# Performance work log

Measured on AMD Instinct MI355X. Metric: run time of the kernel, lower is better.

## Reference

```python
import jax, jax.numpy as jnp
import numpy as np

B, T, DIM, HEADS, DH, MLP = 2, 1024, 768, 8, 96, 3072
EPS = 1e-6


def _rms_norm(x, w):
    return x * jax.lax.rsqrt(jnp.mean(x * x, axis=-1, keepdims=True) + EPS) * w


def _rotate_half(x):
    x1, x2 = jnp.split(x, 2, axis=-1)
    return jnp.concatenate([-x2, x1], axis=-1)


def _l2norm(x):
    n = jnp.sqrt(jnp.sum(x * x, axis=-1, keepdims=True))
    return x / jnp.maximum(n, 1e-12)


def setup_inputs() -> dict:
    key = jax.random.key(0)
    ks = jax.random.split(key, 16)
    def rn(k, shape, s=0.02):
        return jax.random.normal(k, shape, jnp.float32) * s
    return {
        'x_stream1': jax.random.normal(ks[0], (B, T, DIM), jnp.float32),
        'x_stream2': jax.random.normal(ks[1], (B, T, DIM), jnp.float32),
        'p_emb': jax.random.normal(ks[2], (B, 1, 1024), jnp.float32),
        'mod_w1': rn(ks[3], (1024, 512)), 'mod_b1': jnp.zeros((512,), jnp.float32),
        'mod_w2': rn(ks[4], (512, DIM * 12)), 'mod_b2': jnp.zeros((DIM * 12,), jnp.float32),
        'norm11_w': jnp.ones((DIM,), jnp.float32), 'norm12_w': jnp.ones((DIM,), jnp.float32),
        'qkv_w': rn(ks[5], (DIM, 3 * DIM)), 'qkv_b': jnp.zeros((3 * DIM,), jnp.float32),
        'qkv2_w': rn(ks[6], (DIM, 3 * DIM)), 'qkv2_b': jnp.zeros((3 * DIM,), jnp.float32),
        'qk_scale': jnp.full((DH,), 10.0, jnp.float32),
        'out_w': rn(ks[7], (DIM, DIM)), 'out_b': jnp.zeros((DIM,), jnp.float32),
        'norm21_w': jnp.ones((DIM,), jnp.float32), 'norm22_w': jnp.ones((DIM,), jnp.float32),
        'mlp1_w1': rn(ks[8], (DIM, MLP)), 'mlp1_b1': jnp.zeros((MLP,), jnp.float32),
        'mlp1_w2': rn(ks[9], (MLP, DIM)), 'mlp1_b2': jnp.zeros((DIM,), jnp.float32),
        'mlp2_w1': rn(ks[10], (DIM, MLP)), 'mlp2_b1': jnp.zeros((MLP,), jnp.float32),
        'mlp2_w2': rn(ks[11], (MLP, DIM)), 'mlp2_b2': jnp.zeros((DIM,), jnp.float32),
    }


def _forward(x_stream1, x_stream2, p_emb, mod_w1, mod_b1, mod_w2, mod_b2,
             norm11_w, norm12_w, qkv_w, qkv_b, qkv2_w, qkv2_b, qk_scale,
             out_w, out_b, norm21_w, norm22_w,
             mlp1_w1, mlp1_b1, mlp1_w2, mlp1_b2,
             mlp2_w1, mlp2_b1, mlp2_w2, mlp2_b2):
    Bc, Tc, D = x_stream1.shape
    # modulation MLP: SiLU -> Linear -> SiLU -> Linear -> 12 chunks of [B, D]
    h = jax.nn.silu(p_emb[:, 0, :])
    h = jax.nn.silu(h @ mod_w1 + mod_b1)
    mod = h @ mod_w2 + mod_b2
    (m1s, m1h, m1g, m2s, m2h, m2g,
     m3s, m3h, m3g, m4s, m4h, m4g) = [m[:, None, :] for m in jnp.split(mod, 12, axis=1)]

    xm1 = _rms_norm(x_stream1, norm11_w) * (1 + m1s) + m1h
    xm2 = _rms_norm(x_stream2, norm12_w) * (1 + m2s) + m2h

    q1, k1, v1 = jnp.split(xm1 @ qkv_w + qkv_b, 3, axis=-1)
    q2, k2, v2 = jnp.split(xm2 @ qkv2_w + qkv2_b, 3, axis=-1)
    q = jnp.concatenate([q1, q2], axis=1)  # [B, 2T, D]
    k = jnp.concatenate([k1, k2], axis=1)
    v = jnp.concatenate([v1, v2], axis=1)
    N = 2 * Tc

    def to_heads(x):
        return x.reshape(Bc, N, HEADS, DH).transpose(0, 2, 1, 3)  # [B, H, N, dh]
    q, k, v = to_heads(q), to_heads(k), to_heads(v)

    # RoPE (inv_freq computed in bf16 as in the original, then used in fp32)
    inv_freq = (1.0 / (10000.0 ** (jnp.arange(0, DH, 2, dtype=jnp.float32) / DH))).astype(jnp.bfloat16).astype(jnp.float32)
    t = jnp.arange(N, dtype=jnp.float32)
    freqs = t[:, None] * inv_freq[None, :]
    emb = jnp.concatenate([freqs, freqs], axis=-1)  # [N, dh]
    cos, sin = jnp.cos(emb), jnp.sin(emb)
    q = q * cos + _rotate_half(q) * sin
    k = k * cos + _rotate_half(k) * sin

    # QK-Norm
    q = _l2norm(q) * qk_scale
    k = _l2norm(k) * qk_scale

    scores = jnp.einsum('bhid,bhjd->bhij', q, k) * (DH ** -0.5)
    probs = jax.nn.softmax(scores, axis=-1)
    attn = jnp.einsum('bhij,bhjd->bhid', probs, v)
    attn = attn.transpose(0, 2, 1, 3).reshape(Bc, N, D)
    attn = attn @ out_w + out_b

    x1 = x_stream1 + attn[:, :Tc, :] * m1g
    x2 = x_stream2 + attn[:, Tc:, :] * m2g

    xn1 = _rms_norm(x1, norm21_w) * (1 + m3s) + m3h
    mlp1 = jax.nn.gelu(xn1 @ mlp1_w1 + mlp1_b1, approximate=False) @ mlp1_w2 + mlp1_b2
    xn2 = _rms_norm(x2, norm22_w) * (1 + m4s) + m4h
    mlp2 = jax.nn.gelu(xn2 @ mlp2_w1 + mlp2_b1, approximate=False) @ mlp2_w2 + mlp2_b2

    return (x1 + mlp1 * m3g, x2 + mlp2 * m4g)


def reference(x_stream1, x_stream2, p_emb, mod_w1, mod_b1, mod_w2, mod_b2,
              norm11_w, norm12_w, qkv_w, qkv_b, qkv2_w, qkv2_b, qk_scale,
              out_w, out_b, norm21_w, norm22_w,
              mlp1_w1, mlp1_b1, mlp1_w2, mlp1_b2,
              mlp2_w1, mlp2_b1, mlp2_w2, mlp2_b2):
    return _forward(x_stream1, x_stream2, p_emb, mod_w1, mod_b1, mod_w2, mod_b2,
                    norm11_w, norm12_w, qkv_w, qkv_b, qkv2_w, qkv2_b, qk_scale,
                    out_w, out_b, norm21_w, norm22_w,
                    mlp1_w1, mlp1_b1, mlp1_w2, mlp1_b2,
                    mlp2_w1, mlp2_b1, mlp2_w2, mlp2_b2)
```

## Files before the change

kernel.cpp:

```cpp
#include <hip/hip_runtime.h>
#include <hip/hip_bf16.h>
#include <cstdint>
#include <math.h>

#define BB 2
#define TT 1024
#define DIMM 768
#define NHEADS 8
#define DHH 96
#define MLPD 3072
#define NN 2048

typedef unsigned short u16;
using short8 = __attribute__((ext_vector_type(8))) short;
using f32x4  = __attribute__((ext_vector_type(4))) float;
using f32x16 = __attribute__((ext_vector_type(16))) float;
using int4v  = __attribute__((ext_vector_type(4))) int;
union S8I4 { int4v i; short8 s; };

static constexpr float kEps = 1e-6f;

__device__ __forceinline__ float siluf(float x){ return x / (1.f + expf(-x)); }
__device__ __forceinline__ float geluf(float x){ return 0.5f*x*(1.f + erff(x*0.7071067811865475f)); }
__device__ __forceinline__ float bf16_rne(float x){
  uint32_t u = __float_as_uint(x);
  u = (u + 0x7fffu + ((u >> 16) & 1u)) & 0xffff0000u;
  return __uint_as_float(u);
}
__device__ __forceinline__ u16 f2b(float x){
  uint32_t u = __float_as_uint(x);
  return (u16)((u + 0x7fffu + ((u >> 16) & 1u)) >> 16);
}
__device__ __forceinline__ float b2f(u16 b){
  return __uint_as_float(((uint32_t)b) << 16);
}
__device__ __forceinline__ int cvtpk(float lo, float hi){
  int d; asm("v_cvt_pk_bf16_f32 %0, %1, %2" : "=v"(d) : "v"(lo), "v"(hi)); return d;
}
__device__ __forceinline__ void gload16(const void* g, void* l){
  __builtin_amdgcn_global_load_lds((const __attribute__((address_space(1))) unsigned int*)g,
                                   (__attribute__((address_space(3))) unsigned int*)l, 16, 0, 0);
}

__global__ __launch_bounds__(256) void mod_stage1_k(
    const float* __restrict__ p_emb, const float* __restrict__ w1,
    const float* __restrict__ b1, float* __restrict__ h2){
  __shared__ float sp[1024];
  const int b = blockIdx.x >> 1;
  const int obase = (blockIdx.x & 1) * 256;
  for (int i = threadIdx.x; i < 1024; i += 256)
    sp[i] = siluf(p_emb[b*1024 + i]);
  __syncthreads();
  const int o = obase + threadIdx.x;
  float acc = 0.f;
  for (int j = 0; j < 1024; ++j) acc += sp[j] * w1[j*512 + o];
  h2[b*512 + o] = siluf(acc + b1[o]);
}

__global__ __launch_bounds__(256) void mod_stage2_k(
    const float* __restrict__ h2, const float* __restrict__ w2,
    const float* __restrict__ b2, float* __restrict__ mod){
  __shared__ float sh[512];
  const int b = blockIdx.x / 36;
  const int obase = (blockIdx.x % 36) * 256;
  for (int i = threadIdx.x; i < 512; i += 256)
    sh[i] = h2[b*512 + i];
  __syncthreads();
  const int o = obase + threadIdx.x;
  float acc = 0.f;
  for (int j = 0; j < 512; ++j) acc += sh[j] * w2[j*9216 + o];
  mod[b*9216 + o] = acc + b2[o];
}

__global__ __launch_bounds__(256) void wt_all_k(
    const float* __restrict__ s0, u16* __restrict__ d0,
    const float* __restrict__ s1, u16* __restrict__ d1,
    const float* __restrict__ s2, u16* __restrict__ d2,
    const float* __restrict__ s3, u16* __restrict__ d3,
    const float* __restrict__ s4, u16* __restrict__ d4,
    const float* __restrict__ s5, u16* __restrict__ d5,
    const float* __restrict__ s6, u16* __restrict__ d6){
  const int bid = blockIdx.x;
  const float* S; u16* D; int K, N, lid;
  if      (bid < 1728) { S=s0; D=d0; K=768;  N=2304; lid=bid; }
  else if (bid < 3456) { S=s1; D=d1; K=768;  N=2304; lid=bid-1728; }
  else if (bid < 4032) { S=s2; D=d2; K=768;  N=768;  lid=bid-3456; }
  else if (bid < 6336) { S=s3; D=d3; K=768;  N=3072; lid=bid-4032; }
  else if (bid < 8640) { S=s4; D=d4; K=3072; N=768;  lid=bid-6336; }
  else if (bid < 10944){ S=s5; D=d5; K=768;  N=3072; lid=bid-8640; }
  else                 { S=s6; D=d6; K=3072; N=768;  lid=bid-10944; }
  const int nx = N >> 5;
  const int k0 = (lid / nx) * 32, n0 = (lid % nx) * 32;
  __shared__ float t[32][33];
  const int tx = threadIdx.x & 31, ty = threadIdx.x >> 5;
  for (int i = ty; i < 32; i += 8)
    t[i][tx] = S[(size_t)(k0+i)*N + n0 + tx];
  __syncthreads();
  for (int i = ty; i < 32; i += 8)
    D[(size_t)(n0+i)*K + k0 + tx] = f2b(t[tx][i]);
}

__global__ __launch_bounds__(256) void rmsnorm2_k(
    const float* __restrict__ x0, const float* __restrict__ w0, int cs0, int ch0, u16* __restrict__ o0,
    const float* __restrict__ x1, const float* __restrict__ w1, int cs1, int ch1, u16* __restrict__ o1,
    const float* __restrict__ mod){
  const int rowg = blockIdx.x;
  const int s = rowg >> 11;
  const int row = rowg & 2047;
  const float* x = s ? x1 : x0;
  const float* w = s ? w1 : w0;
  const int cs = s ? cs1 : cs0, ch = s ? ch1 : ch0;
  u16* out = s ? o1 : o0;
  const int b = row >> 10;
  const int tid = threadIdx.x;
  const float* xr = x + (size_t)row * DIMM;
  float v0 = xr[tid], v1 = xr[tid + 256], v2 = xr[tid + 512];
  float ss = v0*v0 + v1*v1 + v2*v2;
  __shared__ float red[4];
  for (int m = 1; m < 64; m <<= 1) ss += __shfl_xor(ss, m, 64);
  if ((tid & 63) == 0) red[tid >> 6] = ss;
  __syncthreads();
  float tot = red[0] + red[1] + red[2] + red[3];
  float rms = rsqrtf(tot * (1.f/768.f) + kEps);
  const float* ms = mod + (size_t)b*9216 + (size_t)cs*768;
  const float* mh = mod + (size_t)b*9216 + (size_t)ch*768;
  u16* orow = out + (size_t)row * DIMM;
  orow[tid]       = f2b(v0*rms*w[tid]      *(1.f+ms[tid])       + mh[tid]);
  orow[tid + 256] = f2b(v1*rms*w[tid+256]  *(1.f+ms[tid+256])   + mh[tid+256]);
  orow[tid + 512] = f2b(v2*rms*w[tid+512]  *(1.f+ms[tid+512])   + mh[tid+512]);
}

template<int EPI, int DUAL>
__global__ __launch_bounds__(256) void gemm_bf16_k(
    const u16* __restrict__ A0, const u16* __restrict__ Bt0,
    const float* __restrict__ bias0, void* __restrict__ C0,
    const u16* __restrict__ A1, const u16* __restrict__ Bt1,
    const float* __restrict__ bias1, void* __restrict__ C1,
    const float* __restrict__ mod, const float* __restrict__ X0,
    const float* __restrict__ X1, float* __restrict__ O0,
    float* __restrict__ O1, int cg0, int cg1,
    int M, int N, int K){
  __shared__ u16 As[2][128*32];
  __shared__ u16 Bs[2][128*32];
  const int z = DUAL ? blockIdx.z : 0;
  const u16* A      = z ? A1 : A0;
  const u16* Bt     = z ? Bt1 : Bt0;
  const float* bias = z ? bias1 : bias0;
  void* C           = z ? C1 : C0;
  const int tid = threadIdx.x;
  const int w = tid >> 6, l = tid & 63;
  const int m0 = blockIdx.y*128, n0 = blockIdx.x*128;
  const int wr = w >> 1, wc = w & 1;
  const int la = l & 15, hi4 = l >> 4;
  f32x4 acc[4][4] = {};
  const int nk = K >> 5;
  #pragma unroll
  for (int it = 0; it < 2; ++it){
    const int sb = w*128 + it*64;
    const int s = sb + l;
    const int row = s >> 2, sl = s & 3;
    gload16(A  + (size_t)(m0+row)*K + sl*8, &As[0][sb*8]);
    gload16(Bt + (size_t)(n0+row)*K + sl*8, &Bs[0][sb*8]);
  }
  __syncthreads();
  for (int kt = 0; kt < nk; ++kt){
    const int cur = kt & 1;
    if (kt + 1 < nk){
      const int k0n = (kt+1) << 5;
      #pragma unroll
      for (int it = 0; it < 2; ++it){
        const int sb = w*128 + it*64;
        const int s = sb + l;
        const int row = s >> 2, sl = s & 3;
        gload16(A  + (size_t)(m0+row)*K + k0n + sl*8, &As[cur^1][sb*8]);
        gload16(Bt + (size_t)(n0+row)*K + k0n + sl*8, &Bs[cur^1][sb*8]);
      }
    }
    short8 af[4], bf[4];
    #pragma unroll
    for (int mi = 0; mi < 4; ++mi)
      af[mi] = *(const short8*)((const char*)&As[cur][0] + (wr*64 + mi*16 + la)*64 + hi4*16);
    #pragma unroll
    for (int ni = 0; ni < 4; ++ni)
      bf[ni] = *(const short8*)((const char*)&Bs[cur][0] + (wc*64 + ni*16 + la)*64 + hi4*16);
    #pragma unroll
    for (int mi = 0; mi < 4; ++mi)
      #pragma unroll
      for (int ni = 0; ni < 4; ++ni)
        acc[mi][ni] = __builtin_amdgcn_mfma_f32_16x16x32_bf16(af[mi], bf[ni], acc[mi][ni], 0, 0, 0);
    __syncthreads();
  }
  #pragma unroll
  for (int mi = 0; mi < 4; ++mi){
    #pragma unroll
    for (int ni = 0; ni < 4; ++ni){
      const int n = n0 + wc*64 + ni*16 + la;
      const float bv = bias[n];
      #pragma unroll
      for (int rr = 0; rr < 4; ++rr){
        const int m = m0 + wr*64 + mi*16 + hi4*4 + rr;
        float v = acc[mi][ni][rr] + bv;
        if constexpr (EPI == 2) v = geluf(v);
        if constexpr (EPI == 1 || EPI == 2){
          ((u16*)C)[(size_t)m*N + n] = f2b(v);
        } else if constexpr (EPI == 3){
          const int bb = m >> 11, ss = (m >> 10) & 1, t = m & 1023;
          const float* X = ss ? X1 : X0;
          float* O = ss ? O1 : O0;
          const float g = mod[(size_t)bb*9216 + (size_t)(ss ? cg1 : cg0)*768 + n];
          const size_t oi = ((size_t)(bb*1024 + t))*768 + n;
          O[oi] = X[oi] + v*g;
        } else if constexpr (EPI == 4){
          float* O = z ? O1 : O0;
          const int cg = z ? cg1 : cg0;
          const int bb = m >> 10;
          const float g = mod[(size_t)bb*9216 + (size_t)cg*768 + n];
          O[(size_t)m*N + n] += v*g;
        }
      }
    }
  }
}

__global__ __launch_bounds__(256) void build_qkv_k(
    const u16* __restrict__ qkv1, const u16* __restrict__ qkv2,
    const float* __restrict__ qk_scale,
    u16* __restrict__ Q, u16* __restrict__ K, u16* __restrict__ V){
  const int wid = threadIdx.x >> 6;
  const int lane = threadIdx.x & 63;
  const int row = blockIdx.x * 4 + wid;
  const int n = row & 2047;
  const int h = (row >> 11) & 7;
  const int b = row >> 14;
  const u16* src = (n < TT) ? (qkv1 + ((size_t)b*TT + n) * 2304)
                            : (qkv2 + ((size_t)b*TT + (n - TT)) * 2304);
  const int col = h * DHH;
  const bool act = lane < 48;
  float q0=0,q1=0,k0=0,k1=0,v0=0,v1=0,c=1.f,s=0.f,sc0=0,sc1=0;
  if (act){
    q0 = b2f(src[col + lane]);        q1 = b2f(src[col + lane + 48]);
    k0 = b2f(src[768 + col + lane]);  k1 = b2f(src[768 + col + lane + 48]);
    v0 = b2f(src[1536 + col + lane]); v1 = b2f(src[1536 + col + lane + 48]);
    float inv = bf16_rne((float)(1.0 / pow(10000.0, (2.0 * lane) / 96.0)));
    float ang = (float)n * inv;
    c = cosf(ang); s = sinf(ang);
    sc0 = qk_scale[lane]; sc1 = qk_scale[lane + 48];
  }
  float qr0 = q0*c - q1*s, qr1 = q1*c + q0*s;
  float kr0 = k0*c - k1*s, kr1 = k1*c + k0*s;
  float ssq = qr0*qr0 + qr1*qr1;
  float ssk = kr0*kr0 + kr1*kr1;
  for (int m = 1; m < 64; m <<= 1){ ssq += __shfl_xor(ssq, m, 64); ssk += __shfl_xor(ssk, m, 64); }
  float rq = 1.f / fmaxf(sqrtf(ssq), 1e-12f);
  float rk = 1.f / fmaxf(sqrtf(ssk), 1e-12f);
  const float sscale = 0.1020620726159658f;
  if (act){
    size_t base = (size_t)row * DHH;
    Q[base + lane]      = f2b(qr0*rq*sc0*sscale);  Q[base + lane + 48] = f2b(qr1*rq*sc1*sscale);
    K[base + lane]      = f2b(kr0*rk*sc0);         K[base + lane + 48] = f2b(kr1*rk*sc1);
    V[base + lane]      = f2b(v0);                 V[base + lane + 48] = f2b(v1);
  }
}

__global__ __launch_bounds__(256) void vtrans_k(
    const u16* __restrict__ Vtmp, u16* __restrict__ Vt){
  __shared__ u16 t[32][33];
  const int bh = blockIdx.z;
  const int n0 = blockIdx.x*32, d0 = blockIdx.y*32;
  const int tx = threadIdx.x & 31, ty = threadIdx.x >> 5;
  for (int i = ty; i < 32; i += 8)
    t[i][tx] = Vtmp[((size_t)bh*NN + n0+i)*DHH + d0 + tx];
  __syncthreads();
  for (int i = ty; i < 32; i += 8)
    Vt[((size_t)bh*DHH + d0+i)*NN + n0 + tx] = t[tx][i];
}

#define CROW(r) (((r)&3) + 8*((r)>>2) + 4*hi)
#define SMAXC 10.5f
#define BUILD_PA(dst, vec, basei) { \
  int a1_ = cvtpk(vec[basei+0], vec[basei+1]); \
  int b1_ = cvtpk(vec[basei+4], vec[basei+5]); \
  asm("v_permlane32_swap_b32 %0, %1" : "+v"(a1_), "+v"(b1_)); \
  int a2_ = cvtpk(vec[basei+2], vec[basei+3]); \
  int b2_ = cvtpk(vec[basei+6], vec[basei+7]); \
  asm("v_permlane32_swap_b32 %0, %1" : "+v"(a2_), "+v"(b2_)); \
  S8I4 u_; u_.i = (int4v){a1_, a2_, b1_, b2_}; dst = u_.s; }

__global__ __launch_bounds__(512) void attn_mfma_k(
    const u16* __restrict__ Qg, const u16* __restrict__ Kg,
    const u16* __restrict__ Vtg, u16* __restrict__ AO){
  __shared__ u16 Ks[2][2][64*128];
  __shared__ u16 Vs[2][2][96*64];
  const int bh = blockIdx.x >> 4;
  const int qblk = blockIdx.x & 15;
  const int b = bh >> 3, h = bh & 7;
  const int tid = threadIdx.x;
  const int w = tid >> 6, l = tid & 63;
  const int g2 = w >> 2, wq = w & 3;
  const int gtid = tid & 255;
  const int hi = l >> 5, li = l & 31;
  const int q0w = qblk*128 + wq*32;
  const int kvbase = g2 * 1024;

  short8 qf[6];
  {
    const u16* qrow = Qg + ((size_t)bh*NN + q0w + li)*DHH;
    #pragma unroll
    for (int ks = 0; ks < 6; ++ks)
      qf[ks] = *(const short8*)(qrow + ks*16 + hi*8);
  }

  f32x16 o0, o1, o2;
  #pragma unroll
  for (int r = 0; r < 16; ++r){ o0[r]=0.f; o1[r]=0.f; o2[r]=0.f; }
  float lrun = 0.f;

  {
    #pragma unroll
    for (int it = 0; it < 3; ++it){
      const int s = gtid + it*256;
      const int krow = s/12, ksl = s%12;
      short8 kv = *(const short8*)(Kg + ((size_t)bh*NN + kvbase + krow)*DHH + ksl*8);
      *(short8*)((char*)&Ks[g2][0][0] + krow*256 + ((ksl ^ (krow&7))<<4)) = kv;
      const int vrow = s >> 3, vsl = s & 7;
      short8 vv = *(const short8*)(Vtg + ((size_t)bh*DHH + vrow)*NN + kvbase + vsl*8);
      *(short8*)((char*)&Vs[g2][0][0] + vrow*128 + ((vsl ^ (vrow&7))<<4)) = vv;
    }
  }
  __syncthreads();

  const int NT2 = 16;
  for (int t = 0; t < NT2; ++t){
    const int cur = t & 1;
    short8 kst[3], vst[3];
    if (t + 1 < NT2){
      const int kv0 = kvbase + (t+1)*64;
      #pragma unroll
      for (int it = 0; it < 3; ++it){
        const int s = gtid + it*256;
        const int krow = s/12, ksl = s%12;
        kst[it] = *(const short8*)(Kg + ((size_t)bh*NN + kv0 + krow)*DHH + ksl*8);
        const int vrow = s >> 3, vsl = s & 7;
        vst[it] = *(const short8*)(Vtg + ((size_t)bh*DHH + vrow)*NN + kv0 + vsl*8);
      }
    }
    f32x16 s0, s1;
    #pragma unroll
    for (int r = 0; r < 16; ++r){ s0[r]=0.f; s1[r]=0.f; }
    #pragma unroll
    for (int ks = 0; ks < 6; ++ks){
      const int sl = ks*2 + hi;
      short8 kf0 = *(const short8*)((const char*)&Ks[g2][cur][0] + li*256      + ((sl ^ (li&7))<<4));
      short8 kf1 = *(const short8*)((const char*)&Ks[g2][cur][0] + (32+li)*256 + ((sl ^ ((32+li)&7))<<4));
      s0 = __builtin_amdgcn_mfma_f32_32x32x16_bf16(kf0, qf[ks], s0, 0, 0, 0);
      s1 = __builtin_amdgcn_mfma_f32_32x32x16_bf16(kf1, qf[ks], s1, 0, 0, 0);
    }
    float ps = 0.f;
    #pragma unroll
    for (int r = 0; r < 16; ++r){
      float pa = __expf(s0[r] - SMAXC);
      float pb = __expf(s1[r] - SMAXC);
      s0[r] = pa; s1[r] = pb; ps += pa + pb;
    }
    ps += __shfl_xor(ps, 32);
    lrun += ps;
    short8 pa0, pa1, pa2, pa3;
    BUILD_PA(pa0, s0, 0); BUILD_PA(pa1, s0, 8);
    BUILD_PA(pa2, s1, 0); BUILD_PA(pa3, s1, 8);
    #pragma unroll
    for (int dt = 0; dt < 3; ++dt){
      const int drow = dt*32 + li;
      const char* vb_base = (const char*)&Vs[g2][cur][0] + drow*128;
      f32x16* op = (dt==0)? &o0 : (dt==1)? &o1 : &o2;
      {
        short8 vb = *(const short8*)(vb_base + (((0*2+hi) ^ (drow&7))<<4));
        *op = __builtin_amdgcn_mfma_f32_32x32x16_bf16(pa0, vb, *op, 0, 0, 0);
      }
      {
        short8 vb = *(const short8*)(vb_base + (((1*2+hi) ^ (drow&7))<<4));
        *op = __builtin_amdgcn_mfma_f32_32x32x16_bf16(pa1, vb, *op, 0, 0, 0);
      }
      {
        short8 vb = *(const short8*)(vb_base + (((2*2+hi) ^ (drow&7))<<4));
        *op = __builtin_amdgcn_mfma_f32_32x32x16_bf16(pa2, vb, *op, 0, 0, 0);
      }
      {
        short8 vb = *(const short8*)(vb_base + (((3*2+hi) ^ (drow&7))<<4));
        *op = __builtin_amdgcn_mfma_f32_32x32x16_bf16(pa3, vb, *op, 0, 0, 0);
      }
    }
    __syncthreads();
    if (t + 1 < NT2){
      #pragma unroll
      for (int it = 0; it < 3; ++it){
        const int s = gtid + it*256;
        const int krow = s/12, ksl = s%12;
        *(short8*)((char*)&Ks[g2][cur^1][0] + krow*256 + ((ksl ^ (krow&7))<<4)) = kst[it];
        const int vrow = s >> 3, vsl = s & 7;
        *(short8*)((char*)&Vs[g2][cur^1][0] + vrow*128 + ((vsl ^ (vrow&7))<<4)) = vst[it];
      }
      __syncthreads();
    }
  }

  float* cmb = (float*)&Ks[0][0][0];
  float* cl  = (float*)&Vs[0][0][0];
  if (g2 == 1){
    #pragma unroll
    for (int r = 0; r < 16; ++r){
      cmb[((wq*16 + r)*3 + 0)*64 + l] = o0[r];
      cmb[((wq*16 + r)*3 + 1)*64 + l] = o1[r];
      cmb[((wq*16 + r)*3 + 2)*64 + l] = o2[r];
    }
    if (l < 32) cl[wq*32 + l] = lrun;
  }
  __syncthreads();
  if (g2 == 0){
    #pragma unroll
    for (int r = 0; r < 16; ++r){
      o0[r] += cmb[((wq*16 + r)*3 + 0)*64 + l];
      o1[r] += cmb[((wq*16 + r)*3 + 1)*64 + l];
      o2[r] += cmb[((wq*16 + r)*3 + 2)*64 + l];
    }
    lrun += cl[wq*32 + li];
    const float linv = 1.f / lrun;
    #pragma unroll
    for (int r = 0; r < 16; ++r){
      const float lr = __shfl(linv, CROW(r), 64);
      const int n = q0w + CROW(r);
      u16* dst = AO + ((size_t)b*NN + n)*DIMM + h*DHH + li;
      dst[0]  = f2b(o0[r]*lr);
      dst[32] = f2b(o1[r]*lr);
      dst[64] = f2b(o2[r]*lr);
    }
  }
}

static constexpr size_t W_QKV1T = 0;
static constexpr size_t W_QKV2T = W_QKV1T + 3538944;
static constexpr size_t W_OUTT  = W_QKV2T + 3538944;
static constexpr size_t W_M1W1T = W_OUTT  + 1179648;
static constexpr size_t W_M1W2T = W_M1W1T + 4718592;
static constexpr size_t W_M2W1T = W_M1W2T + 4718592;
static constexpr size_t W_M2W2T = W_M2W1T + 4718592;
static constexpr size_t O_MODH  = W_M2W2T + 4718592;
static constexpr size_t O_MODB  = O_MODH + 4096;
static constexpr size_t DYN     = O_MODB + 73728;
static constexpr size_t O_XM1   = DYN;
static constexpr size_t O_XM2   = O_XM1 + 3145728;
static constexpr size_t O_QKV1  = O_XM2 + 3145728;
static constexpr size_t O_QKV2  = O_QKV1 + 9437184;
static constexpr size_t O_QB    = O_QKV2 + 9437184;
static constexpr size_t O_KB    = O_QB + 6291456;
static constexpr size_t O_VTMP  = O_KB + 6291456;
static constexpr size_t O_PF    = O_VTMP + 6291456;
static constexpr size_t O_VT    = O_QKV1;
static constexpr size_t O_AO    = O_QKV2;
static constexpr size_t O_H1    = O_QB;
static constexpr size_t O_H2    = O_PF;

extern "C" void kernel_launch(void* const* d_in, const int* in_sizes, int n_in,
                              void* d_out, int out_size, void* d_ws, size_t ws_size,
                              hipStream_t stream){
  const float* x_s1   = (const float*)d_in[0];
  const float* x_s2   = (const float*)d_in[1];
  const float* p_emb  = (const float*)d_in[2];
  const float* mod_w1 = (const float*)d_in[3];
  const float* mod_b1 = (const float*)d_in[4];
  const float* mod_w2 = (const float*)d_in[5];
  const float* mod_b2 = (const float*)d_in[6];
  const float* n11_w  = (const float*)d_in[7];
  const float* n12_w  = (const float*)d_in[8];
  const float* qkv_w  = (const float*)d_in[9];
  const float* qkv_b  = (const float*)d_in[10];
  const float* qkv2_w = (const float*)d_in[11];
  const float* qkv2_b = (const float*)d_in[12];
  const float* qk_sc  = (const float*)d_in[13];
  const float* out_w  = (const float*)d_in[14];
  const float* out_b  = (const float*)d_in[15];
  const float* n21_w  = (const float*)d_in[16];
  const float* n22_w  = (const float*)d_in[17];
  const float* m1w1   = (const float*)d_in[18];
  const float* m1b1   = (const float*)d_in[19];
  const float* m1w2   = (const float*)d_in[20];
  const float* m1b2   = (const float*)d_in[21];
  const float* m2w1   = (const float*)d_in[22];
  const float* m2b1   = (const float*)d_in[23];
  const float* m2w2   = (const float*)d_in[24];
  const float* m2b2   = (const float*)d_in[25];

  char* ws = (char*)d_ws;
  u16* qkv1t = (u16*)(ws + W_QKV1T);
  u16* qkv2t = (u16*)(ws + W_QKV2T);
  u16* outt  = (u16*)(ws + W_OUTT);
  u16* w11t  = (u16*)(ws + W_M1W1T);
  u16* w12t  = (u16*)(ws + W_M1W2T);
  u16* w21t  = (u16*)(ws + W_M2W1T);
  u16* w22t  = (u16*)(ws + W_M2W2T);
  float* h2b  = (float*)(ws + O_MODH);
  float* modb = (float*)(ws + O_MODB);
  u16* xm1  = (u16*)(ws + O_XM1);
  u16* xm2  = (u16*)(ws + O_XM2);
  u16* qkv1 = (u16*)(ws + O_QKV1);
  u16* qkv2 = (u16*)(ws + O_QKV2);
  u16* Qb   = (u16*)(ws + O_QB);
  u16* Kb   = (u16*)(ws + O_KB);
  u16* Vtmp = (u16*)(ws + O_VTMP);
  u16* Vt   = (u16*)(ws + O_VT);
  u16* AO   = (u16*)(ws + O_AO);
  u16* H1   = (u16*)(ws + O_H1);
  u16* H2   = (u16*)(ws + O_H2);

  float* out0 = (float*)d_out;
  float* out1 = out0 + (size_t)BB*TT*DIMM;

  wt_all_k<<<13248, 256, 0, stream>>>(qkv_w, qkv1t, qkv2_w, qkv2t, out_w, outt,
                                      m1w1, w11t, m1w2, w12t, m2w1, w21t, m2w2, w22t);

  mod_stage1_k<<<4, 256, 0, stream>>>(p_emb, mod_w1, mod_b1, h2b);
  mod_stage2_k<<<72, 256, 0, stream>>>(h2b, mod_w2, mod_b2, modb);

  rmsnorm2_k<<<2*BB*TT, 256, 0, stream>>>(x_s1, n11_w, 0, 1, xm1,
                                          x_s2, n12_w, 3, 4, xm2, modb);

  gemm_bf16_k<1,1><<<dim3(18, 16, 2), 256, 0, stream>>>(
      xm1, qkv1t, qkv_b, qkv1, xm2, qkv2t, qkv2_b, qkv2,
      nullptr, nullptr, nullptr, nullptr, nullptr, 0, 0, 2048, 2304, 768);

  build_qkv_k<<<(BB*NHEADS*NN)/4, 256, 0, stream>>>(qkv1, qkv2, qk_sc, Qb, Kb, Vtmp);

  vtrans_k<<<dim3(NN/32, DHH/32, 16), 256, 0, stream>>>(Vtmp, Vt);

  attn_mfma_k<<<16*16, 512, 0, stream>>>(Qb, Kb, Vt, AO);

  gemm_bf16_k<3,0><<<dim3(6, 32, 1), 256, 0, stream>>>(
      AO, outt, out_b, nullptr, AO, outt, out_b, nullptr,
      modb, x_s1, x_s2, out0, out1, 2, 5, 4096, 768, 768);

  rmsnorm2_k<<<2*BB*TT, 256, 0, stream>>>(out0, n21_w, 6, 7, xm1,
                                          out1, n22_w, 9, 10, xm2, modb);

  gemm_bf16_k<2,1><<<dim3(24, 16, 2), 256, 0, stream>>>(
      xm1, w11t, m1b1, H1, xm2, w21t, m2b1, H2,
      nullptr, nullptr, nullptr, nullptr, nullptr, 0, 0, 2048, 3072, 768);

  gemm_bf16_k<4,1><<<dim3(6, 16, 2), 256, 0, stream>>>(
      H1, w12t, m1b2, nullptr, H2, w22t, m2b2, nullptr,
      modb, nullptr, nullptr, out0, out1, 8, 11, 2048, 768, 3072);
}
```

Baseline: 309.6 us.

## Split-K within a block for the narrow output GEMMs with LDS reduction

After: 280.0 us. 9.6% less time.

```diff
diff --git a/kernel.cpp b/kernel.cpp
--- a/kernel.cpp
+++ b/kernel.cpp
@@ -136,9 +136,6 @@
     const float* __restrict__ bias0, void* __restrict__ C0,
     const u16* __restrict__ A1, const u16* __restrict__ Bt1,
     const float* __restrict__ bias1, void* __restrict__ C1,
-    const float* __restrict__ mod, const float* __restrict__ X0,
-    const float* __restrict__ X1, float* __restrict__ O0,
-    float* __restrict__ O1, int cg0, int cg1,
     int M, int N, int K){
   __shared__ u16 As[2][128*32];
   __shared__ u16 Bs[2][128*32];
@@ -201,25 +198,132 @@
         const int m = m0 + wr*64 + mi*16 + hi4*4 + rr;
         float v = acc[mi][ni][rr] + bv;
         if constexpr (EPI == 2) v = geluf(v);
-        if constexpr (EPI == 1 || EPI == 2){
-          ((u16*)C)[(size_t)m*N + n] = f2b(v);
-        } else if constexpr (EPI == 3){
-          const int bb = m >> 11, ss = (m >> 10) & 1, t = m & 1023;
-          const float* X = ss ? X1 : X0;
-          float* O = ss ? O1 : O0;
-          const float g = mod[(size_t)bb*9216 + (size_t)(ss ? cg1 : cg0)*768 + n];
-          const size_t oi = ((size_t)(bb*1024 + t))*768 + n;
-          O[oi] = X[oi] + v*g;
-        } else if constexpr (EPI == 4){
-          float* O = z ? O1 : O0;
-          const int cg = z ? cg1 : cg0;
-          const int bb = m >> 10;
-          const float g = mod[(size_t)bb*9216 + (size_t)cg*768 + n];
-          O[(size_t)m*N + n] += v*g;
+        ((u16*)C)[(size_t)m*N + n] = f2b(v);
+      }
+    }
+  }
+}
+
+template<int EPI, int DUAL>
+__global__ __launch_bounds__(1024) void gemm16_k(
+    const u16* __restrict__ A0, const u16* __restrict__ Bt0,
+    const float* __restrict__ bias0,
+    const u16* __restrict__ A1, const u16* __restrict__ Bt1,
+    const float* __restrict__ bias1,
+    const float* __restrict__ mod, const float* __restrict__ X0,
+    const float* __restrict__ X1, float* __restrict__ O0,
+    float* __restrict__ O1, int cg0, int cg1,
+    int M, int N, int K){
+  __shared__ char lds[131072];
+  const int bid = blockIdx.x;
+  const int xcd = bid & 7, kk = bid >> 3;
+  const int g = xcd + 8*(kk/6);
+  const int x = kk % 6;
+  int by, z;
+  if constexpr (DUAL){ by = g & 15; z = g >> 4; } else { by = g; z = 0; }
+  const u16* A      = z ? A1 : A0;
+  const u16* Bt     = z ? Bt1 : Bt0;
+  const float* bias = z ? bias1 : bias0;
+  const int tid = threadIdx.x;
+  const int w = tid >> 6, l = tid & 63;
+  const int kg = w >> 2, gw = w & 3;
+  const int m0 = by*128, n0 = x*128;
+  const int wr = gw >> 1, wc = gw & 1;
+  const int la = l & 15, hi4 = l >> 4;
+  u16* AsG = (u16*)(lds + kg*32768);
+  u16* BsG = (u16*)(lds + kg*32768 + 16384);
+  const int Kg = K >> 2;
+  const int nk = Kg >> 5;
+  const int kbase = kg * Kg;
+  f32x4 acc[4][4] = {};
+  #pragma unroll
+  for (int it = 0; it < 2; ++it){
+    const int sb = gw*128 + it*64;
+    const int s = sb + l;
+    const int row = s >> 2, sl = s & 3;
+    gload16(A  + (size_t)(m0+row)*K + kbase + sl*8, AsG + sb*8);
+    gload16(Bt + (size_t)(n0+row)*K + kbase + sl*8, BsG + sb*8);
+  }
+  __syncthreads();
+  for (int kt = 0; kt < nk; ++kt){
+    const int cur = kt & 1;
+    if (kt + 1 < nk){
+      const int k0n = kbase + ((kt+1) << 5);
+      #pragma unroll
+      for (int it = 0; it < 2; ++it){
+        const int sb = gw*128 + it*64;
+        const int s = sb + l;
+        const int row = s >> 2, sl = s & 3;
+        gload16(A  + (size_t)(m0+row)*K + k0n + sl*8, AsG + (cur^1)*4096 + sb*8);
+        gload16(Bt + (size_t)(n0+row)*K + k0n + sl*8, BsG + (cur^1)*4096 + sb*8);
+      }
+    }
+    short8 af[4], bf[4];
+    #pragma unroll
+    for (int mi = 0; mi < 4; ++mi)
+      af[mi] = *(const short8*)(AsG + cur*4096 + (wr*64 + mi*16 + la)*32 + hi4*8);
+    #pragma unroll
+    for (int ni = 0; ni < 4; ++ni)
+      bf[ni] = *(const short8*)(BsG + cur*4096 + (wc*64 + ni*16 + la)*32 + hi4*8);
+    #pragma unroll
+    for (int mi = 0; mi < 4; ++mi)
+      #pragma unroll
+      for (int ni = 0; ni < 4; ++ni)
+        acc[mi][ni] = __builtin_amdgcn_mfma_f32_16x16x32_bf16(af[mi], bf[ni], acc[mi][ni], 0, 0, 0);
+    __syncthreads();
+  }
+  float* c0 = (float*)lds;
+  float* c1 = (float*)(lds + 65536);
+  #define WRACC(cb) { \
+    _Pragma("unroll") for (int mi = 0; mi < 4; ++mi) \
+    _Pragma("unroll") for (int ni = 0; ni < 4; ++ni) \
+    _Pragma("unroll") for (int rr = 0; rr < 4; ++rr) \
+      (cb)[(wr*64+mi*16+hi4*4+rr)*128 + wc*64+ni*16+la] = acc[mi][ni][rr]; }
+  #define RDACC(cb) { \
+    _Pragma("unroll") for (int mi = 0; mi < 4; ++mi) \
+    _Pragma("unroll") for (int ni = 0; ni < 4; ++ni) \
+    _Pragma("unroll") for (int rr = 0; rr < 4; ++rr) \
+      acc[mi][ni][rr] += (cb)[(wr*64+mi*16+hi4*4+rr)*128 + wc*64+ni*16+la]; }
+  if (kg == 1) WRACC(c0);
+  if (kg == 3) WRACC(c1);
+  __syncthreads();
+  if (kg == 0) RDACC(c0);
+  if (kg == 2) RDACC(c1);
+  __syncthreads();
+  if (kg == 2) WRACC(c0);
+  __syncthreads();
+  if (kg == 0){
+    RDACC(c0);
+    #pragma unroll
+    for (int mi = 0; mi < 4; ++mi){
+      #pragma unroll
+      for (int ni = 0; ni < 4; ++ni){
+        const int n = n0 + wc*64 + ni*16 + la;
+        const float bv = bias[n];
+        #pragma unroll
+        for (int rr = 0; rr < 4; ++rr){
+          const int m = m0 + wr*64 + mi*16 + hi4*4 + rr;
+          float v = acc[mi][ni][rr] + bv;
+          if constexpr (EPI == 3){
+            const int bb = m >> 11, ss = (m >> 10) & 1, t = m & 1023;
+            const float* X = ss ? X1 : X0;
+            float* O = ss ? O1 : O0;
+            const float gmod = mod[(size_t)bb*9216 + (size_t)(ss ? cg1 : cg0)*768 + n];
+            const size_t oi = ((size_t)(bb*1024 + t))*768 + n;
+            O[oi] = X[oi] + v*gmod;
+          } else {
+            float* O = z ? O1 : O0;
+            const int cg = z ? cg1 : cg0;
+            const int bb = m >> 10;
+            const float gmod = mod[(size_t)bb*9216 + (size_t)cg*768 + n];
+            O[(size_t)m*N + n] += v*gmod;
+          }
         }
       }
     }
   }
+  #undef WRACC
+  #undef RDACC
 }
 
 __global__ __launch_bounds__(256) void build_qkv_k(
@@ -524,8 +628,7 @@
                                           x_s2, n12_w, 3, 4, xm2, modb);
 
   gemm_bf16_k<1,1><<<dim3(18, 16, 2), 256, 0, stream>>>(
-      xm1, qkv1t, qkv_b, qkv1, xm2, qkv2t, qkv2_b, qkv2,
-      nullptr, nullptr, nullptr, nullptr, nullptr, 0, 0, 2048, 2304, 768);
+      xm1, qkv1t, qkv_b, qkv1, xm2, qkv2t, qkv2_b, qkv2, 2048, 2304, 768);
 
   build_qkv_k<<<(BB*NHEADS*NN)/4, 256, 0, stream>>>(qkv1, qkv2, qk_sc, Qb, Kb, Vtmp);
 
@@ -533,18 +636,17 @@
 
   attn_mfma_k<<<16*16, 512, 0, stream>>>(Qb, Kb, Vt, AO);
 
-  gemm_bf16_k<3,0><<<dim3(6, 32, 1), 256, 0, stream>>>(
-      AO, outt, out_b, nullptr, AO, outt, out_b, nullptr,
+  gemm16_k<3,0><<<192, 1024, 0, stream>>>(
+      AO, outt, out_b, AO, outt, out_b,
       modb, x_s1, x_s2, out0, out1, 2, 5, 4096, 768, 768);
 
   rmsnorm2_k<<<2*BB*TT, 256, 0, stream>>>(out0, n21_w, 6, 7, xm1,
                                           out1, n22_w, 9, 10, xm2, modb);
 
   gemm_bf16_k<2,1><<<dim3(24, 16, 2), 256, 0, stream>>>(
-      xm1, w11t, m1b1, H1, xm2, w21t, m2b1, H2,
-      nullptr, nullptr, nullptr, nullptr, nullptr, 0, 0, 2048, 3072, 768);
-
-  gemm_bf16_k<4,1><<<dim3(6, 16, 2), 256, 0, stream>>>(
-      H1, w12t, m1b2, nullptr, H2, w22t, m2b2, nullptr,
+      xm1, w11t, m1b1, H1, xm2, w21t, m2b1, H2, 2048, 3072, 768);
+
+  gemm16_k<4,1><<<192, 1024, 0, stream>>>(
+      H1, w12t, m1b2, H2, w22t, m2b2,
       modb, nullptr, nullptr, out0, out1, 8, 11, 2048, 768, 3072);
 }
```
